# Performance work log

Measured on AMD Instinct MI355X. Metric: run time of the kernel, lower is better.

The kernel has to match this reference:

```python
import jax, jax.numpy as jnp
import numpy as np

K = 16  # from init_kwargs

def setup_inputs() -> dict:
    key = jax.random.key(0)
    inputs = jax.random.normal(key, (16384, 128), dtype=jnp.float32)
    return {"inputs": inputs}

def reference(inputs) -> jnp.ndarray:
    # Pairwise Euclidean distances (torch.cdist, p=2): [N, N]
    sq = jnp.sum(inputs * inputs, axis=1)  # [N]
    d2 = sq[:, None] + sq[None, :] - 2.0 * (inputs @ inputs.T)
    dist = jnp.sqrt(jnp.maximum(d2, 0.0))
    # Original does a full sort per row then slices indices[:, 1:k+1].
    # top_k of (k+1) smallest is the equivalent math without the full sort.
    _, idx = jax.lax.top_k(-dist, K + 1)  # [N, K+1], ascending distance
    return idx[:, 1:]  # drop self (distance 0), [N, K] int32
```

## Files before the change

kernel.cpp:

```cpp
#include <hip/hip_runtime.h>
#include <hip/hip_bf16.h>
#include <math.h>

#define NPTS    16384
#define DIM     128
#define KSEL    16
#define TSEL    18
#define NSC     8
#define RPB     32
#define THREADS 256
#define NT      ((NPTS / 2) / 16)
#define RESC    32
#define SKSTR   145
#define NC      (NSC * TSEL)
#define CSTRIDE 145
#define IDXMASK 0x3FFFu

typedef float f32x4  __attribute__((ext_vector_type(4)));
typedef short bf16x8 __attribute__((ext_vector_type(8)));

__device__ __forceinline__ unsigned short f2b(float f) {
    __hip_bfloat16 h = __float2bfloat16(f);
    return *(unsigned short*)&h;
}

#define MED3_LADDER(bv, val)                                   \
    do {                                                       \
        _Pragma("unroll")                                      \
        for (int k = TSEL - 1; k >= 1; --k)                    \
            bv[k] = fminf(bv[k], fmaxf(bv[k - 1], (val)));     \
        bv[0] = fminf(bv[0], (val));                           \
    } while (0)

__device__ __forceinline__ float packkey(float val, int jg) {
    const unsigned int u =
        (__float_as_uint(val) & 0xFFFFC000u) | (unsigned int)(jg & 0x3FFF);
    return __uint_as_float(u);
}

__device__ __forceinline__ float np_sq_avx512(const float* __restrict__ x) {
    float s[16];
    #pragma unroll
    for (int L = 0; L < 16; ++L) {
        const float m0 = __fmul_rn(x[  0 + L], x[  0 + L]);
        const float m1 = __fmul_rn(x[ 16 + L], x[ 16 + L]);
        const float m2 = __fmul_rn(x[ 32 + L], x[ 32 + L]);
        const float m3 = __fmul_rn(x[ 48 + L], x[ 48 + L]);
        const float m4 = __fmul_rn(x[ 64 + L], x[ 64 + L]);
        const float m5 = __fmul_rn(x[ 80 + L], x[ 80 + L]);
        const float m6 = __fmul_rn(x[ 96 + L], x[ 96 + L]);
        const float m7 = __fmul_rn(x[112 + L], x[112 + L]);
        s[L] = __fadd_rn(
            __fadd_rn(__fadd_rn(m0, m1), __fadd_rn(m2, m3)),
            __fadd_rn(__fadd_rn(m4, m5), __fadd_rn(m6, m7)));
    }
    float u[8];
    #pragma unroll
    for (int i = 0; i < 8; ++i) u[i] = __fadd_rn(s[i], s[i + 8]);
    float v[4];
    #pragma unroll
    for (int i = 0; i < 4; ++i) v[i] = __fadd_rn(u[i], u[i + 4]);
    return __fadd_rn(__fadd_rn(v[0], v[2]), __fadd_rn(v[1], v[3]));
}

__device__ __forceinline__ float scan_sq(const float* __restrict__ xp) {
    const float4* x4 = (const float4*)xp;
    float a0 = 0.f, a1 = 0.f, a2 = 0.f, a3 = 0.f;
    #pragma unroll
    for (int g = 0; g < 32; ++g) {
        const float4 b = x4[g];
        a0 += b.x * b.x; a1 += b.y * b.y;
        a2 += b.z * b.z; a3 += b.w * b.w;
    }
    return (a0 + a1) + (a2 + a3);
}

__global__ __launch_bounds__(256)
void sq_kernel(const float* __restrict__ X, float* __restrict__ sqws) {
    const int j = blockIdx.x * 256 + threadIdx.x;
    sqws[j] = 0.5f * scan_sq(X + (size_t)j * DIM);
}

__global__ __launch_bounds__(256)
void cvt_kernel(const float* __restrict__ X, unsigned short* __restrict__ Xb) {
    const size_t i = ((size_t)blockIdx.x * 256 + threadIdx.x) * 8;
    const float4 v0 = *(const float4*)(X + i);
    const float4 v1 = *(const float4*)(X + i + 4);
    ushort4 o0, o1;
    o0.x = f2b(v0.x); o0.y = f2b(v0.y); o0.z = f2b(v0.z); o0.w = f2b(v0.w);
    o1.x = f2b(v1.x); o1.y = f2b(v1.y); o1.z = f2b(v1.z); o1.w = f2b(v1.w);
    *(ushort4*)(Xb + i) = o0;
    *(ushort4*)(Xb + i + 4) = o1;
}

__global__ __launch_bounds__(THREADS, 2)
void knn_packed(const float* __restrict__ X, const float* __restrict__ sqws,
                const unsigned short* __restrict__ Xb, int* __restrict__ out) {
    __shared__ __align__(16) char smem[30848];
    float*              sk = (float*)smem;
    unsigned int*       ci = (unsigned int*)(smem + 18560);
    unsigned long long* ek = (unsigned long long*)(smem + 22656);

    const int tid  = threadIdx.x;
    const int w    = tid >> 6;
    const int l    = tid & 63;
    const int lg   = l >> 4;
    const int l15  = l & 15;
    const int rloc = (w >> 1) * 16 + l15;
    const int grow = blockIdx.x * RPB + rloc;
    const int colbase = (w & 1) * (NPTS / 2);
    const int sid = (w & 1) * 4 + lg;

    bf16x8 nb[4];
    {
        const unsigned short* xr = Xb + (size_t)grow * DIM + lg * 8;
        #pragma unroll
        for (int m = 0; m < 4; ++m) {
            union { bf16x8 h; uint4 u; } t;
            t.h = *(const bf16x8*)(xr + m * 32);
            t.u.x ^= 0x80008000u; t.u.y ^= 0x80008000u;
            t.u.z ^= 0x80008000u; t.u.w ^= 0x80008000u;
            nb[m] = t.h;
        }
    }

    float bv[TSEL];
    #pragma unroll
    for (int k = 0; k < TSEL; ++k) bv[k] = 3.0e38f;
    {
        const unsigned short* ap = Xb + (size_t)(colbase + l15) * DIM + lg * 8;
        #pragma unroll 1
        for (int t = 0; t < NT; t += 2) {
            const int cb = colbase + t * 16;
            const bf16x8 a0 = *(const bf16x8*)(ap);
            const bf16x8 a1 = *(const bf16x8*)(ap + 32);
            const bf16x8 a2 = *(const bf16x8*)(ap + 64);
            const bf16x8 a3 = *(const bf16x8*)(ap + 96);
            const bf16x8 b0 = *(const bf16x8*)(ap + 16 * DIM);
            const bf16x8 b1 = *(const bf16x8*)(ap + 16 * DIM + 32);
            const bf16x8 b2 = *(const bf16x8*)(ap + 16 * DIM + 64);
            const bf16x8 b3 = *(const bf16x8*)(ap + 16 * DIM + 96);
            ap += 32 * DIM;
            f32x4 aA1 = *(const f32x4*)&sqws[cb + lg * 4];
            f32x4 aA2 = {0.f, 0.f, 0.f, 0.f};
            f32x4 aB1 = *(const f32x4*)&sqws[cb + 16 + lg * 4];
            f32x4 aB2 = {0.f, 0.f, 0.f, 0.f};
            aA1 = __builtin_amdgcn_mfma_f32_16x16x32_bf16(a0, nb[0], aA1, 0, 0, 0);
            aA2 = __builtin_amdgcn_mfma_f32_16x16x32_bf16(a2, nb[2], aA2, 0, 0, 0);
            aB1 = __builtin_amdgcn_mfma_f32_16x16x32_bf16(b0, nb[0], aB1, 0, 0, 0);
            aB2 = __builtin_amdgcn_mfma_f32_16x16x32_bf16(b2, nb[2], aB2, 0, 0, 0);
            aA1 = __builtin_amdgcn_mfma_f32_16x16x32_bf16(a1, nb[1], aA1, 0, 0, 0);
            aA2 = __builtin_amdgcn_mfma_f32_16x16x32_bf16(a3, nb[3], aA2, 0, 0, 0);
            aB1 = __builtin_amdgcn_mfma_f32_16x16x32_bf16(b1, nb[1], aB1, 0, 0, 0);
            aB2 = __builtin_amdgcn_mfma_f32_16x16x32_bf16(b3, nb[3], aB2, 0, 0, 0);
            #pragma unroll
            for (int r = 0; r < 4; ++r) {
                const float pA = packkey(aA1[r] + aA2[r], cb + lg * 4 + r);
                MED3_LADDER(bv, pA);
            }
            #pragma unroll
            for (int r = 0; r < 4; ++r) {
                const float pB = packkey(aB1[r] + aB2[r], cb + 16 + lg * 4 + r);
                MED3_LADDER(bv, pB);
            }
        }
    }

    #pragma unroll
    for (int k = 0; k < TSEL; ++k)
        sk[rloc * SKSTR + sid * TSEL + k] = bv[k];
    __syncthreads();

    if (tid < RPB) {
        const int base = tid * SKSTR;
        int head[NSC];
        #pragma unroll
        for (int s2 = 0; s2 < NSC; ++s2) head[s2] = 0;
        for (int m = 0; m < RESC; ++m) {
            float best = 3.0e38f; int bs = 0;
            #pragma unroll
            for (int s2 = 0; s2 < NSC; ++s2) {
                const float v = (head[s2] < TSEL)
                    ? sk[base + s2 * TSEL + head[s2]] : 3.0e38f;
                if (v < best) { best = v; bs = s2; }
            }
            ci[tid * RESC + m] = __float_as_uint(best) & IDXMASK;
            #pragma unroll
            for (int s2 = 0; s2 < NSC; ++s2) head[s2] += (s2 == bs) ? 1 : 0;
        }
    }
    __syncthreads();

    float4 xi4[32];
    {
        const float4* xr = (const float4*)(X + (size_t)grow * DIM);
        #pragma unroll
        for (int g = 0; g < 32; ++g) xi4[g] = xr[g];
    }
    const float sqi32 = np_sq_avx512(X + (size_t)grow * DIM);

    #pragma unroll 1
    for (int q = 0; q < RESC / NSC; ++q) {
        const int m = sid * (RESC / NSC) + q;
        const int j = (int)ci[rloc * RESC + m];
        unsigned long long key;
        if (j == grow) {
            key = 0xFFFFFFFFFFFFFFFFULL;
        } else {
            const float* xjp = X + (size_t)j * DIM;
            const float4* xj = (const float4*)xjp;
            const float sqj32 = np_sq_avx512(xjp);
            float cacc = 0.f;
            #pragma unroll
            for (int g = 0; g < 32; ++g) {
                const float4 a = xi4[g], b = xj[g];
                cacc = __fmaf_rn(a.x, b.x, cacc);
                cacc = __fmaf_rn(a.y, b.y, cacc);
                cacc = __fmaf_rn(a.z, b.z, cacc);
                cacc = __fmaf_rn(a.w, b.w, cacc);
            }
            float d2c = __fsub_rn(__fadd_rn(sqi32, sqj32),
                                  __fmul_rn(2.0f, cacc));
            if (d2c < 0.0f) d2c = 0.0f;
            const float dist32 = sqrtf(d2c);
            key = ((unsigned long long)__float_as_uint(dist32) << 32)
                  | (unsigned int)j;
        }
        ek[rloc * RESC + m] = key;
    }
    __syncthreads();

    if (tid < RPB) {
        const int base = tid * RESC;
        const int i = blockIdx.x * RPB + tid;
        for (int m = 0; m < KSEL; ++m) {
            unsigned long long best = 0xFFFFFFFFFFFFFFFFULL; int bc = 0;
            for (int c2 = 0; c2 < RESC; ++c2) {
                const unsigned long long v = ek[base + c2];
                if (v < best) { best = v; bc = c2; }
            }
            out[(size_t)i * KSEL + m] = (int)(best & 0xFFFFFFFFULL);
            ek[base + bc] = 0xFFFFFFFFFFFFFFFFULL;
        }
    }
}

__global__ __launch_bounds__(THREADS, 2)
void knn_mono(const float* __restrict__ X, int* __restrict__ out) {
    __shared__ __align__(16) char smem[NPTS * 4];
    float* sqh = (float*)smem;
    unsigned long long* keys = (unsigned long long*)smem;
    const int tid = threadIdx.x;
    const int w = tid >> 6, l = tid & 63, lg = l >> 4, l15 = l & 15;
    const int rloc = (w >> 1) * 16 + l15;
    const int grow = blockIdx.x * RPB + rloc;
    const int colbase = (w & 1) * (NPTS / 2);
    const int s = (w & 1) * 4 + lg;
    #pragma unroll 1
    for (int q = 0; q < NPTS / THREADS; ++q) {
        const int j = tid + THREADS * q;
        sqh[j] = 0.5f * scan_sq(X + (size_t)j * DIM);
    }
    __syncthreads();
    bf16x8 nb[4];
    {
        const float* xr = X + (size_t)grow * DIM + lg * 8;
        #pragma unroll
        for (int m = 0; m < 4; ++m) {
            bf16x8 h;
            #pragma unroll
            for (int e = 0; e < 8; ++e) h[e] = (short)f2b(-xr[m * 32 + e]);
            nb[m] = h;
        }
    }
    float bv[TSEL]; int bi[TSEL];
    #pragma unroll
    for (int k = 0; k < TSEL; ++k) { bv[k] = 3.0e38f; bi[k] = 0; }
    const float* apf = X + (size_t)(colbase + l15) * DIM + lg * 8;
    #pragma unroll 1
    for (int t = 0; t < NT; ++t) {
        const int cb = colbase + t * 16;
        bf16x8 a0, a1, a2, a3;
        #pragma unroll
        for (int e = 0; e < 8; ++e) {
            a0[e] = (short)f2b(apf[e]);
            a1[e] = (short)f2b(apf[32 + e]);
            a2[e] = (short)f2b(apf[64 + e]);
            a3[e] = (short)f2b(apf[96 + e]);
        }
        apf += 16 * DIM;
        f32x4 acc = *(const f32x4*)&sqh[cb + lg * 4];
        acc = __builtin_amdgcn_mfma_f32_16x16x32_bf16(a0, nb[0], acc, 0, 0, 0);
        acc = __builtin_amdgcn_mfma_f32_16x16x32_bf16(a1, nb[1], acc, 0, 0, 0);
        acc = __builtin_amdgcn_mfma_f32_16x16x32_bf16(a2, nb[2], acc, 0, 0, 0);
        acc = __builtin_amdgcn_mfma_f32_16x16x32_bf16(a3, nb[3], acc, 0, 0, 0);
        #pragma unroll
        for (int r = 0; r < 4; ++r) {
            const float val = acc[r];
            if (val < bv[TSEL - 1]) {
                const int jg = cb + lg * 4 + r;
                #pragma unroll
                for (int k = TSEL - 1; k >= 1; --k) {
                    const bool m1 = val < bv[k - 1];
                    const bool m2 = val < bv[k];
                    bv[k] = m1 ? bv[k - 1] : (m2 ? val : bv[k]);
                    bi[k] = m1 ? bi[k - 1] : (m2 ? jg  : bi[k]);
                }
                if (val < bv[0]) { bv[0] = val; bi[0] = jg; }
            }
        }
    }
    __syncthreads();
    float4 xi4[32];
    {
        const float4* xr = (const float4*)(X + (size_t)grow * DIM);
        #pragma unroll
        for (int g = 0; g < 32; ++g) xi4[g] = xr[g];
    }
    const float sqi32 = np_sq_avx512(X + (size_t)grow * DIM);
    #pragma unroll
    for (int k = 0; k < TSEL; ++k) {
        const int j = bi[k];
        unsigned long long key;
        if (j == grow) {
            key = 0xFFFFFFFFFFFFFFFFULL;
        } else {
            const float* xjp = X + (size_t)j * DIM;
            const float4* xj = (const float4*)xjp;
            const float sqj32 = np_sq_avx512(xjp);
            float cacc = 0.f;
            #pragma unroll
            for (int g = 0; g < 32; ++g) {
                const float4 a = xi4[g], b = xj[g];
                cacc = __fmaf_rn(a.x, b.x, cacc);
                cacc = __fmaf_rn(a.y, b.y, cacc);
                cacc = __fmaf_rn(a.z, b.z, cacc);
                cacc = __fmaf_rn(a.w, b.w, cacc);
            }
            float d2c = __fsub_rn(__fadd_rn(sqi32, sqj32),
                                  __fmul_rn(2.0f, cacc));
            if (d2c < 0.0f) d2c = 0.0f;
            const float dist32 = sqrtf(d2c);
            key = ((unsigned long long)__float_as_uint(dist32) << 32)
                  | (unsigned int)j;
        }
        keys[rloc * CSTRIDE + s * TSEL + k] = key;
    }
    __syncthreads();
    if (tid < RPB) {
        const int base = tid * CSTRIDE;
        const int i = blockIdx.x * RPB + tid;
        for (int m = 0; m < KSEL; ++m) {
            unsigned long long best = 0xFFFFFFFFFFFFFFFFULL; int bc = 0;
            for (int c2 = 0; c2 < NC; ++c2) {
                const unsigned long long v = keys[base + c2];
                if (v < best) { best = v; bc = c2; }
            }
            out[(size_t)i * KSEL + m] = (int)(best & 0xFFFFFFFFULL);
            keys[base + bc] = 0xFFFFFFFFFFFFFFFFULL;
        }
    }
}

extern "C" void kernel_launch(void* const* d_in, const int* in_sizes, int n_in,
                              void* d_out, int out_size, void* d_ws, size_t ws_size,
                              hipStream_t stream) {
    (void)in_sizes; (void)n_in; (void)out_size;
    const float* X = (const float*)d_in[0];
    int* out = (int*)d_out;
    const size_t WS_NEED = (size_t)NPTS * 4 + (size_t)NPTS * DIM * 2;
    if (ws_size >= WS_NEED) {
        float* sqws = (float*)d_ws;
        unsigned short* Xb = (unsigned short*)((char*)d_ws + (size_t)NPTS * 4);
        sq_kernel<<<dim3(NPTS / 256), dim3(256), 0, stream>>>(X, sqws);
        cvt_kernel<<<dim3(NPTS * DIM / 8 / 256), dim3(256), 0, stream>>>(X, Xb);
        knn_packed<<<dim3(NPTS / RPB), dim3(THREADS), 0, stream>>>(X, sqws, Xb, out);
    } else {
        knn_mono<<<dim3(NPTS / RPB), dim3(THREADS), 0, stream>>>(X, out);
    }
}
```

Measured before the change: 607.6 us.

## Split scan into column-quarter blocks and separate fp32 rescoring kernel

```diff
diff --git a/kernel.cpp b/kernel.cpp
--- a/kernel.cpp
+++ b/kernel.cpp
@@ -6,14 +6,15 @@
 #define DIM     128
 #define KSEL    16
 #define TSEL    18
-#define NSC     8
 #define RPB     32
 #define THREADS 256
-#define NT      ((NPTS / 2) / 16)
+#define QSEL    20
+#define NQ      4
+#define NRC     (NQ * QSEL)
+#define SKQ     145
+#define NC      (8 * TSEL)
+#define CSTRIDE 145
 #define RESC    32
-#define SKSTR   145
-#define NC      (NSC * TSEL)
-#define CSTRIDE 145
 #define IDXMASK 0x3FFFu
 
 typedef float f32x4  __attribute__((ext_vector_type(4)));
@@ -93,6 +94,151 @@
     *(ushort4*)(Xb + i + 4) = o1;
 }
 
+__global__ __launch_bounds__(THREADS, 3)
+void scan_q(const float* __restrict__ sqws,
+            const unsigned short* __restrict__ Xb,
+            unsigned short* __restrict__ candw) {
+    __shared__ float sk[RPB * SKQ];
+
+    const int tid  = threadIdx.x;
+    const int w    = tid >> 6;
+    const int l    = tid & 63;
+    const int lg   = l >> 4;
+    const int l15  = l & 15;
+    const int rg   = w >> 1;
+    const int st   = w & 1;
+    const int rb   = blockIdx.x >> 2;
+    const int qq   = blockIdx.x & 3;
+    const int rloc = rg * 16 + l15;
+    const int grow = rb * RPB + rloc;
+    const int colbase = qq * (NPTS / 4) + st * (NPTS / 8);
+    const int sid  = st * 4 + lg;
+
+    bf16x8 nb[4];
+    {
+        const unsigned short* xr = Xb + (size_t)grow * DIM + lg * 8;
+        #pragma unroll
+        for (int m = 0; m < 4; ++m) {
+            union { bf16x8 h; uint4 u; } t;
+            t.h = *(const bf16x8*)(xr + m * 32);
+            t.u.x ^= 0x80008000u; t.u.y ^= 0x80008000u;
+            t.u.z ^= 0x80008000u; t.u.w ^= 0x80008000u;
+            nb[m] = t.h;
+        }
+    }
+
+    float bv[TSEL];
+    #pragma unroll
+    for (int k = 0; k < TSEL; ++k) bv[k] = 3.0e38f;
+    {
+        const unsigned short* ap = Xb + (size_t)(colbase + l15) * DIM + lg * 8;
+        #pragma unroll 1
+        for (int t = 0; t < (NPTS / 8) / 16; ++t) {
+            const int cb = colbase + t * 16;
+            const bf16x8 a0 = *(const bf16x8*)(ap);
+            const bf16x8 a1 = *(const bf16x8*)(ap + 32);
+            const bf16x8 a2 = *(const bf16x8*)(ap + 64);
+            const bf16x8 a3 = *(const bf16x8*)(ap + 96);
+            ap += 16 * DIM;
+            f32x4 acc1 = *(const f32x4*)&sqws[cb + lg * 4];
+            f32x4 acc2 = {0.f, 0.f, 0.f, 0.f};
+            acc1 = __builtin_amdgcn_mfma_f32_16x16x32_bf16(a0, nb[0], acc1, 0, 0, 0);
+            acc2 = __builtin_amdgcn_mfma_f32_16x16x32_bf16(a2, nb[2], acc2, 0, 0, 0);
+            acc1 = __builtin_amdgcn_mfma_f32_16x16x32_bf16(a1, nb[1], acc1, 0, 0, 0);
+            acc2 = __builtin_amdgcn_mfma_f32_16x16x32_bf16(a3, nb[3], acc2, 0, 0, 0);
+            #pragma unroll
+            for (int r = 0; r < 4; ++r) {
+                const float p = packkey(acc1[r] + acc2[r], cb + lg * 4 + r);
+                MED3_LADDER(bv, p);
+            }
+        }
+    }
+
+    #pragma unroll
+    for (int k = 0; k < TSEL; ++k)
+        sk[rloc * SKQ + sid * TSEL + k] = bv[k];
+    __syncthreads();
+
+    if (tid < RPB) {
+        const int base = tid * SKQ;
+        const int row = rb * RPB + tid;
+        unsigned short* po = candw + ((size_t)row * NQ + qq) * QSEL;
+        int head[8];
+        #pragma unroll
+        for (int s2 = 0; s2 < 8; ++s2) head[s2] = 0;
+        for (int m = 0; m < QSEL; ++m) {
+            float best = 3.0e38f; int bs = 0;
+            #pragma unroll
+            for (int s2 = 0; s2 < 8; ++s2) {
+                const float v = (head[s2] < TSEL)
+                    ? sk[base + s2 * TSEL + head[s2]] : 3.0e38f;
+                if (v < best) { best = v; bs = s2; }
+            }
+            po[m] = (unsigned short)(__float_as_uint(best) & IDXMASK);
+            #pragma unroll
+            for (int s2 = 0; s2 < 8; ++s2) head[s2] += (s2 == bs) ? 1 : 0;
+        }
+    }
+}
+
+__global__ __launch_bounds__(THREADS)
+void rescore_f(const float* __restrict__ X,
+               const unsigned short* __restrict__ candw,
+               int* __restrict__ out) {
+    __shared__ unsigned long long ek[4][NRC];
+
+    const int tid  = threadIdx.x;
+    const int rw   = tid >> 6;
+    const int lane = tid & 63;
+    const int row  = blockIdx.x * 4 + rw;
+
+    const float* xip = X + (size_t)row * DIM;
+    const float4* xi4g = (const float4*)xip;
+    const float sqi32 = np_sq_avx512(xip);
+
+    #pragma unroll 1
+    for (int m = lane; m < NRC; m += 64) {
+        const int j = (int)candw[(size_t)row * NRC + m];
+        unsigned long long key;
+        if (j == row) {
+            key = 0xFFFFFFFFFFFFFFFFULL;
+        } else {
+            const float* xjp = X + (size_t)j * DIM;
+            const float4* xj = (const float4*)xjp;
+            const float sqj32 = np_sq_avx512(xjp);
+            float cacc = 0.f;
+            #pragma unroll
+            for (int g = 0; g < 32; ++g) {
+                const float4 a = xi4g[g], b = xj[g];
+                cacc = __fmaf_rn(a.x, b.x, cacc);
+                cacc = __fmaf_rn(a.y, b.y, cacc);
+                cacc = __fmaf_rn(a.z, b.z, cacc);
+                cacc = __fmaf_rn(a.w, b.w, cacc);
+            }
+            float d2c = __fsub_rn(__fadd_rn(sqi32, sqj32),
+                                  __fmul_rn(2.0f, cacc));
+            if (d2c < 0.0f) d2c = 0.0f;
+            const float dist32 = sqrtf(d2c);
+            key = ((unsigned long long)__float_as_uint(dist32) << 32)
+                  | (unsigned int)j;
+        }
+        ek[rw][m] = key;
+    }
+    __syncthreads();
+
+    if (lane == 0) {
+        for (int m = 0; m < KSEL; ++m) {
+            unsigned long long best = 0xFFFFFFFFFFFFFFFFULL; int bc = 0;
+            for (int c2 = 0; c2 < NRC; ++c2) {
+                const unsigned long long v = ek[rw][c2];
+                if (v < best) { best = v; bc = c2; }
+            }
+            out[(size_t)row * KSEL + m] = (int)(best & 0xFFFFFFFFULL);
+            ek[rw][bc] = 0xFFFFFFFFFFFFFFFFULL;
+        }
+    }
+}
+
 __global__ __launch_bounds__(THREADS, 2)
 void knn_packed(const float* __restrict__ X, const float* __restrict__ sqws,
                 const unsigned short* __restrict__ Xb, int* __restrict__ out) {
@@ -130,7 +276,7 @@
     {
         const unsigned short* ap = Xb + (size_t)(colbase + l15) * DIM + lg * 8;
         #pragma unroll 1
-        for (int t = 0; t < NT; t += 2) {
+        for (int t = 0; t < (NPTS / 2) / 16; t += 2) {
             const int cb = colbase + t * 16;
             const bf16x8 a0 = *(const bf16x8*)(ap);
             const bf16x8 a1 = *(const bf16x8*)(ap + 32);
@@ -168,25 +314,25 @@
 
     #pragma unroll
     for (int k = 0; k < TSEL; ++k)
-        sk[rloc * SKSTR + sid * TSEL + k] = bv[k];
+        sk[rloc * SKQ + sid * TSEL + k] = bv[k];
     __syncthreads();
 
     if (tid < RPB) {
-        const int base = tid * SKSTR;
-        int head[NSC];
-        #pragma unroll
-        for (int s2 = 0; s2 < NSC; ++s2) head[s2] = 0;
+        const int base = tid * SKQ;
+        int head[8];
+        #pragma unroll
+        for (int s2 = 0; s2 < 8; ++s2) head[s2] = 0;
         for (int m = 0; m < RESC; ++m) {
             float best = 3.0e38f; int bs = 0;
             #pragma unroll
-            for (int s2 = 0; s2 < NSC; ++s2) {
+            for (int s2 = 0; s2 < 8; ++s2) {
                 const float v = (head[s2] < TSEL)
                     ? sk[base + s2 * TSEL + head[s2]] : 3.0e38f;
                 if (v < best) { best = v; bs = s2; }
             }
             ci[tid * RESC + m] = __float_as_uint(best) & IDXMASK;
             #pragma unroll
-            for (int s2 = 0; s2 < NSC; ++s2) head[s2] += (s2 == bs) ? 1 : 0;
+            for (int s2 = 0; s2 < 8; ++s2) head[s2] += (s2 == bs) ? 1 : 0;
         }
     }
     __syncthreads();
@@ -200,8 +346,8 @@
     const float sqi32 = np_sq_avx512(X + (size_t)grow * DIM);
 
     #pragma unroll 1
-    for (int q = 0; q < RESC / NSC; ++q) {
-        const int m = sid * (RESC / NSC) + q;
+    for (int q = 0; q < RESC / 8; ++q) {
+        const int m = sid * (RESC / 8) + q;
         const int j = (int)ci[rloc * RESC + m];
         unsigned long long key;
         if (j == grow) {
@@ -278,7 +424,7 @@
     for (int k = 0; k < TSEL; ++k) { bv[k] = 3.0e38f; bi[k] = 0; }
     const float* apf = X + (size_t)(colbase + l15) * DIM + lg * 8;
     #pragma unroll 1
-    for (int t = 0; t < NT; ++t) {
+    for (int t = 0; t < (NPTS / 2) / 16; ++t) {
         const int cb = colbase + t * 16;
         bf16x8 a0, a1, a2, a3;
         #pragma unroll
@@ -368,10 +514,18 @@
     (void)in_sizes; (void)n_in; (void)out_size;
     const float* X = (const float*)d_in[0];
     int* out = (int*)d_out;
-    const size_t WS_NEED = (size_t)NPTS * 4 + (size_t)NPTS * DIM * 2;
-    if (ws_size >= WS_NEED) {
-        float* sqws = (float*)d_ws;
-        unsigned short* Xb = (unsigned short*)((char*)d_ws + (size_t)NPTS * 4);
+    const size_t sqB   = (size_t)NPTS * 4;
+    const size_t xbB   = (size_t)NPTS * DIM * 2;
+    const size_t candB = (size_t)NPTS * NRC * 2;
+    float* sqws = (float*)d_ws;
+    unsigned short* Xb = (unsigned short*)((char*)d_ws + sqB);
+    unsigned short* candw = (unsigned short*)((char*)d_ws + sqB + xbB);
+    if (ws_size >= sqB + xbB + candB) {
+        sq_kernel<<<dim3(NPTS / 256), dim3(256), 0, stream>>>(X, sqws);
+        cvt_kernel<<<dim3(NPTS * DIM / 8 / 256), dim3(256), 0, stream>>>(X, Xb);
+        scan_q<<<dim3((NPTS / RPB) * NQ), dim3(THREADS), 0, stream>>>(sqws, Xb, candw);
+        rescore_f<<<dim3(NPTS / 4), dim3(THREADS), 0, stream>>>(X, candw, out);
+    } else if (ws_size >= sqB + xbB) {
         sq_kernel<<<dim3(NPTS / 256), dim3(256), 0, stream>>>(X, sqws);
         cvt_kernel<<<dim3(NPTS * DIM / 8 / 256), dim3(256), 0, stream>>>(X, Xb);
         knn_packed<<<dim3(NPTS / RPB), dim3(THREADS), 0, stream>>>(X, sqws, Xb, out);
```

Measured after the change: 929.4 us. +53.0%, slower.
